# Kernel optimization log

Hardware: AMD Instinct MI355X
Metric: run time of the kernel (lower is better)

Reference implementation:

```python
import jax, jax.numpy as jnp
import numpy as np

V, E, H, K, B, T = 50000, 256, 128, 32, 64, 512


def lstm_dir(x, Wih, Whh, b, reverse):
    # x: [B,T,D]; torch gate order i,f,g,o
    Bsz = x.shape[0]
    xs = jnp.einsum('btd,gd->btg', x, Wih) + b  # [B,T,4H] precomputed input proj
    xs = jnp.swapaxes(xs, 0, 1)                 # [T,B,4H]
    def step(carry, xt):
        h, c = carry
        g = xt + h @ Whh.T
        i, f, gg, o = jnp.split(g, 4, axis=-1)
        c = jax.nn.sigmoid(f) * c + jax.nn.sigmoid(i) * jnp.tanh(gg)
        h = jax.nn.sigmoid(o) * jnp.tanh(c)
        return (h, c), h
    init = (jnp.zeros((Bsz, H), x.dtype), jnp.zeros((Bsz, H), x.dtype))
    _, hs = jax.lax.scan(step, init, xs, reverse=reverse)
    return jnp.swapaxes(hs, 0, 1)  # [B,T,H], time order preserved


def bilstm(x, layer_params):
    h = x
    for (Wf, Uf, bf, Wb, Ub, bb) in layer_params:
        fwd = lstm_dir(h, Wf, Uf, bf, False)
        bwd = lstm_dir(h, Wb, Ub, bb, True)
        h = jnp.concatenate([fwd, bwd], axis=-1)
    return h  # [B,T,2H]


def crf_nll(emissions, tags, mask, trans, start, end):
    Bsz, Tlen, Kn = emissions.shape
    maskf = mask.astype(emissions.dtype)
    # --- forward algorithm (log partition) ---
    alpha0 = start[None, :] + emissions[:, 0]  # [B,K]
    def step(alpha, xt):
        emit_t, m_t = xt  # [B,K], [B]
        score = alpha[:, :, None] + trans[None, :, :] + emit_t[:, None, :]  # [B,K,K]
        new = jax.nn.logsumexp(score, axis=1)
        alpha = jnp.where(m_t[:, None], new, alpha)
        return alpha, None
    em_t = jnp.swapaxes(emissions[:, 1:], 0, 1)  # [T-1,B,K]
    mk_t = jnp.swapaxes(mask[:, 1:], 0, 1)       # [T-1,B]
    alpha, _ = jax.lax.scan(step, alpha0, (em_t, mk_t))
    logZ = jax.nn.logsumexp(alpha + end[None, :], axis=1)  # [B]
    # --- gold path score ---
    emit = jnp.take_along_axis(emissions, tags[:, :, None].astype(jnp.int32), axis=2)[..., 0]  # [B,T]
    tr = trans[tags[:, 1:], tags[:, :-1]]  # [B,T-1]
    gold = start[tags[:, 0]] + emit[:, 0] + jnp.sum((emit[:, 1:] + tr) * maskf[:, 1:], axis=1)
    last = mask.astype(jnp.int32).sum(1) - 1
    last_tags = jnp.take_along_axis(tags, last[:, None], axis=1)[:, 0]
    gold = gold + end[last_tags]
    return jnp.mean(logZ - gold)


def setup_inputs() -> dict:
    key = jax.random.key(0)
    ks = jax.random.split(key, 24)
    s = 1.0 / np.sqrt(H)
    u = lambda k, sh, sc: jax.random.uniform(k, sh, jnp.float32, -sc, sc)
    inp = {}
    inp['x'] = jax.random.randint(ks[0], (B, T), 1, V, dtype=jnp.int32)  # avoid pad_idx 0
    inp['lens'] = jnp.full((B,), T, dtype=jnp.int32)
    inp['tags'] = jax.random.randint(ks[1], (B, T), 0, K, dtype=jnp.int32)
    inp['mask'] = jnp.ones((B, T), dtype=bool)
    emb = jax.random.normal(ks[2], (V, E), jnp.float32) * 0.1
    inp['emb'] = emb.at[0].set(0.0)  # padding_idx row
    d_in = [E, 2 * H]
    i = 3
    for l in range(2):
        for dname in ('f', 'b'):
            inp[f'Wih_l{l}{dname}'] = u(ks[i], (4 * H, d_in[l]), s); i += 1
            inp[f'Whh_l{l}{dname}'] = u(ks[i], (4 * H, H), s); i += 1
            inp[f'b_l{l}{dname}'] = u(ks[i], (4 * H,), s); i += 1  # bih+bhh combined
    inp['fcW'] = u(ks[i], (K, 2 * H), 1.0 / np.sqrt(2 * H)); i += 1
    inp['fcb'] = u(ks[i], (K,), 1.0 / np.sqrt(2 * H)); i += 1
    inp['trans'] = jax.random.normal(ks[i + 1], (K, K), jnp.float32) * 0.01
    inp['start'] = jax.random.normal(ks[i + 2], (K,), jnp.float32) * 0.01
    inp['end'] = jax.random.normal(ks[i + 3], (K,), jnp.float32) * 0.01
    return inp


def reference(x, lens, tags, mask, emb,
              Wih_l0f, Whh_l0f, b_l0f, Wih_l0b, Whh_l0b, b_l0b,
              Wih_l1f, Whh_l1f, b_l1f, Wih_l1b, Whh_l1b, b_l1b,
              fcW, fcb, trans, start, end):
    layer_params = [(Wih_l0f, Whh_l0f, b_l0f, Wih_l0b, Whh_l0b, b_l0b),
                    (Wih_l1f, Whh_l1f, b_l1f, Wih_l1b, Whh_l1b, b_l1b)]
    e = emb[x]                      # [B,T,E]
    o = bilstm(e, layer_params)     # [B,T,2H] (dropout: eval mode -> identity)
    emissions = o @ fcW.T + fcb     # [B,T,K]
    return crf_nll(emissions, tags, mask, trans, start, end)
```

## Files before the change

kernel.cpp:

```cpp
#include <hip/hip_runtime.h>
#include <stddef.h>

typedef unsigned short u16;
typedef unsigned int u32;

#define DEV __device__ __forceinline__

constexpr int Bb = 64;
constexpr int Tt = 512;
constexpr int Ee = 256;
constexpr int Hh = 128;
constexpr int Kk = 32;
constexpr int G4 = 4 * Hh;
constexpr int BT = Bb * Tt;

DEV u16 f2b(float f) {
  u32 u = __builtin_bit_cast(u32, f);
  u += 0x7fffu + ((u >> 16) & 1u);
  return (u16)(u >> 16);
}
DEV float b2f(u16 v) { return __builtin_bit_cast(float, (u32)v << 16); }
DEV float rcp_(float x) { float r; asm("v_rcp_f32 %0, %1" : "=v"(r) : "v"(x)); return r; }
DEV float sigmoidf_(float x) { return rcp_(1.0f + __expf(-x)); }
DEV float tanhf_(float x) { return 1.0f - 2.0f * rcp_(1.0f + __expf(2.0f * x)); }

DEV void gload16(const void* g, void* l) {
  __builtin_amdgcn_global_load_lds(
      (const __attribute__((address_space(1))) void*)g,
      (__attribute__((address_space(3))) void*)l, 16, 0, 0);
}

DEV void lds_barrier() {
  asm volatile("s_waitcnt lgkmcnt(0)" ::: "memory");
  __builtin_amdgcn_sched_barrier(0);
  __builtin_amdgcn_s_barrier();
  __builtin_amdgcn_sched_barrier(0);
}

__global__ __launch_bounds__(256) void k_embprep(
    const int* __restrict__ x, const float* __restrict__ emb,
    u16* __restrict__ eout,
    const float* __restrict__ W0, const float* __restrict__ W1,
    const float* __restrict__ W2, const float* __restrict__ W3,
    u16* __restrict__ d0, u16* __restrict__ d1,
    u16* __restrict__ d2, u16* __restrict__ d3,
    const float* __restrict__ fcW, u16* __restrict__ fcwb,
    const float* __restrict__ bi0, const float* __restrict__ bi1,
    const float* __restrict__ bi2, const float* __restrict__ bi3,
    float* __restrict__ bias_p) {
  int blk = blockIdx.x, tid = threadIdx.x;
  if (blk < 8192) {
    int m = blk * 4 + (tid >> 6);
    int lane = tid & 63;
    int b = m & 63, t = m >> 6;
    int idx = x[b * Tt + t];
    float4 v = ((const float4*)(emb + (size_t)idx * Ee))[lane];
    uint2 p;
    p.x = (u32)f2b(v.x) | ((u32)f2b(v.y) << 16);
    p.y = (u32)f2b(v.z) | ((u32)f2b(v.w) << 16);
    ((uint2*)(eout + (size_t)m * Ee))[lane] = p;
    return;
  }
  blk -= 8192;
  if (blk < 512) {
    int a = blk >> 7;
    const float* s; u16* d;
    if (a == 0)      { s = W0; d = d0; }
    else if (a == 1) { s = W1; d = d1; }
    else if (a == 2) { s = W2; d = d2; }
    else             { s = W3; d = d3; }
    int i = (blk & 127) * 256 + tid;
    int np = i >> 6, k4 = i & 63;
    int src = (np & 3) * 128 + (np >> 2);
    float4 v = ((const float4*)(s + (size_t)src * 256))[k4];
    uint2 p;
    p.x = (u32)f2b(v.x) | ((u32)f2b(v.y) << 16);
    p.y = (u32)f2b(v.z) | ((u32)f2b(v.w) << 16);
    ((uint2*)(d + (size_t)np * 256))[k4] = p;
  } else if (blk < 520) {
    int i = (blk - 512) * 256 + tid;
    float4 v = ((const float4*)fcW)[i];
    uint2 p;
    p.x = (u32)f2b(v.x) | ((u32)f2b(v.y) << 16);
    p.y = (u32)f2b(v.z) | ((u32)f2b(v.w) << 16);
    ((uint2*)fcwb)[i] = p;
  } else {
    int i = (blk - 520) * 256 + tid;
    int a = i >> 9, np = i & 511;
    const float* s;
    if (a == 0)      s = bi0;
    else if (a == 1) s = bi1;
    else if (a == 2) s = bi2;
    else             s = bi3;
    bias_p[i] = s[(np & 3) * 128 + (np >> 2)];
  }
}

typedef __attribute__((ext_vector_type(8))) short bfrag;
typedef __attribute__((ext_vector_type(4))) float ffrag;

__global__ __launch_bounds__(256) void k_gemm5(const u16* __restrict__ X,
                                               const u16* __restrict__ Wp0,
                                               const u16* __restrict__ Wp1,
                                               const float* __restrict__ bp0,
                                               const float* __restrict__ bp1,
                                               u16* __restrict__ out0,
                                               u16* __restrict__ out1) {
  __shared__ __align__(16) u16 Xs[128 * 64];
  __shared__ __align__(16) u16 Ws[128 * 64];
  const int tid = threadIdx.x;
  const int bm = blockIdx.x * 128;
  const int sel = blockIdx.y >> 2;
  const int bnp = (blockIdx.y & 3) * 128;
  const u16* __restrict__ Wp = sel ? Wp1 : Wp0;
  const float* __restrict__ bp = sel ? bp1 : bp0;
  u16* __restrict__ outp = sel ? out1 : out0;
  const int w = tid >> 6;
  const int l = tid & 63;
  const int r16 = l & 15;
  const int q = l >> 4;
  const int wrN = (w >> 1) * 64;
  const int wcM = (w & 1) * 64;

  const int srow = l >> 3;
  const int scol = l & 7;

  ffrag acc[4][4];
#pragma unroll
  for (int i = 0; i < 4; ++i)
#pragma unroll
    for (int jn = 0; jn < 4; ++jn) acc[i][jn] = (ffrag)0.0f;

  for (int kt = 0; kt < 256; kt += 64) {
#pragma unroll
    for (int i = 0; i < 4; ++i) {
      int row = w * 32 + i * 8 + srow;
      int gcol = (scol ^ (row & 7)) << 3;
      gload16(&X[(size_t)(bm + row) * 256 + kt + gcol], &Xs[(w * 32 + i * 8) * 64]);
      gload16(&Wp[(size_t)(bnp + row) * 256 + kt + gcol], &Ws[(w * 32 + i * 8) * 64]);
    }
    __syncthreads();
#pragma unroll
    for (int kk = 0; kk < 2; ++kk) {
      bfrag af[4], bf[4];
#pragma unroll
      for (int fm = 0; fm < 4; ++fm) {
        int row = wrN + fm * 16 + r16;
        int ck = (kk * 4 + q) ^ (row & 7);
        af[fm] = *(const bfrag*)&Ws[row * 64 + ck * 8];
      }
#pragma unroll
      for (int fn = 0; fn < 4; ++fn) {
        int row = wcM + fn * 16 + r16;
        int ck = (kk * 4 + q) ^ (row & 7);
        bf[fn] = *(const bfrag*)&Xs[row * 64 + ck * 8];
      }
#pragma unroll
      for (int fm = 0; fm < 4; ++fm)
#pragma unroll
        for (int fn = 0; fn < 4; ++fn)
          acc[fm][fn] = __builtin_amdgcn_mfma_f32_16x16x32_bf16(
              af[fm], bf[fn], acc[fm][fn], 0, 0, 0);
    }
    __syncthreads();
  }
  const int Q = l >> 4;
#pragma unroll
  for (int fm = 0; fm < 4; ++fm) {
    int np0 = bnp + wrN + fm * 16 + 4 * Q;
    int j = np0 >> 2;
    float4 bv = *(const float4*)&bp[np0];
#pragma unroll
    for (int fn = 0; fn < 4; ++fn) {
      int m = bm + wcM + fn * 16 + r16;
      int t = m >> 6, bq = (m & 63) >> 2;
      size_t flat = ((size_t)t * 16 + bq) * 2048 + (size_t)j * 16 + (m & 3) * 4;
      float v0 = acc[fm][fn][0] + bv.x, v1 = acc[fm][fn][1] + bv.y;
      float v2 = acc[fm][fn][2] + bv.z, v3 = acc[fm][fn][3] + bv.w;
      u32 lo, hi;
      asm("v_cvt_pk_bf16_f32 %0, %1, %2" : "=v"(lo) : "v"(v0), "v"(v1));
      asm("v_cvt_pk_bf16_f32 %0, %1, %2" : "=v"(hi) : "v"(v2), "v"(v3));
      uint2 st; st.x = lo; st.y = hi;
      *(uint2*)&outp[flat] = st;
    }
  }
}

__global__ __launch_bounds__(512, 1) void k_lstm9(const u16* __restrict__ xpf,
                                                  const u16* __restrict__ xpb,
                                                  const float* __restrict__ whhf,
                                                  const float* __restrict__ whhb,
                                                  u16* __restrict__ out) {
  __shared__ u16 hbuf[2][4][128];
  const int dir = blockIdx.x >> 4;
  const int wg = blockIdx.x & 15;
  const u16* __restrict__ xp = dir ? xpb : xpf;
  const float* __restrict__ whh = dir ? whhb : whhf;
  const int tid = threadIdx.x;
  const int w = tid >> 6;
  const int l = tid & 63;
  const int q = l >> 4;
  const int jw = l & 15;
  const int j = 16 * w + jw;

  for (int i = tid; i < 2 * 4 * 128; i += 512) (&hbuf[0][0][0])[i] = 0;

  bfrag wf[4][4];
#pragma unroll
  for (int g = 0; g < 4; ++g) {
    const float* rowp = whh + (size_t)(g * 128 + j) * 128;
#pragma unroll
    for (int ks = 0; ks < 4; ++ks) {
      float4 x0 = ((const float4*)(rowp + ks * 32 + q * 8))[0];
      float4 x1 = ((const float4*)(rowp + ks * 32 + q * 8))[1];
      bfrag t;
      t[0] = (short)f2b(x0.x); t[1] = (short)f2b(x0.y);
      t[2] = (short)f2b(x0.z); t[3] = (short)f2b(x0.w);
      t[4] = (short)f2b(x1.x); t[5] = (short)f2b(x1.y);
      t[6] = (short)f2b(x1.z); t[7] = (short)f2b(x1.w);
      wf[g][ks] = t;
    }
  }
  __syncthreads();

  const int dt = dir ? -1 : 1;
  const int tp0 = dir ? (Tt - 1) : 0;
  const size_t xoff = (size_t)wg * 2048 + (size_t)j * 16 + (size_t)q * 4;
  float cc = 0.f;
  int cur = 0;
  u16 hprev = 0;

  const bool ld_act = ((jw & 3) == 0);
  const int drow = jw >> 2;
  const int rsw = (drow & 1) << 5;
  const int wsw = (q & 1) << 5;
  bfrag hf0 = (bfrag)(short)0, hf1 = (bfrag)(short)0;
  bfrag hf2 = (bfrag)(short)0, hf3 = (bfrag)(short)0;

  uint2 xv[4];
#pragma unroll
  for (int d = 0; d < 4; ++d)
    xv[d] = *(const uint2*)&xp[(size_t)(tp0 + d * dt) * 32768 + xoff];

  const ptrdiff_t xstep = (ptrdiff_t)dt * 32768;
  const u16* pxq = xp + (size_t)(tp0 + 4 * dt) * 32768 + xoff;
  u16* optr = out + ((size_t)tp0 * 64 + 4 * wg + q) * 256 + (size_t)dir * 128 + j;
  const ptrdiff_t ostep = (ptrdiff_t)dt * 16384;

  for (int it = 0; it < Tt / 4; ++it) {
#pragma unroll
    for (int d = 0; d < 4; ++d) {
      if (it > 0 || d > 0) { *optr = hprev; optr += ostep; }

      if (ld_act) {
        const u16* hb = &hbuf[cur][drow][0];
        hf0 = *(const bfrag*)&hb[(0 * 32 + q * 8) ^ rsw];
        hf1 = *(const bfrag*)&hb[(1 * 32 + q * 8) ^ rsw];
        hf2 = *(const bfrag*)&hb[(2 * 32 + q * 8) ^ rsw];
        hf3 = *(const bfrag*)&hb[(3 * 32 + q * 8) ^ rsw];
      }

      ffrag a0 = __builtin_amdgcn_mfma_f32_16x16x32_bf16(hf0, wf[0][0], (ffrag)0.f, 0, 0, 0);
      ffrag a1 = __builtin_amdgcn_mfma_f32_16x16x32_bf16(hf0, wf[1][0], (ffrag)0.f, 0, 0, 0);
      ffrag a2 = __builtin_amdgcn_mfma_f32_16x16x32_bf16(hf0, wf[2][0], (ffrag)0.f, 0, 0, 0);
      ffrag a3 = __builtin_amdgcn_mfma_f32_16x16x32_bf16(hf0, wf[3][0], (ffrag)0.f, 0, 0, 0);
      a0 = __builtin_amdgcn_mfma_f32_16x16x32_bf16(hf1, wf[0][1], a0, 0, 0, 0);
      a1 = __builtin_amdgcn_mfma_f32_16x16x32_bf16(hf1, wf[1][1], a1, 0, 0, 0);
      a2 = __builtin_amdgcn_mfma_f32_16x16x32_bf16(hf1, wf[2][1], a2, 0, 0, 0);
      a3 = __builtin_amdgcn_mfma_f32_16x16x32_bf16(hf1, wf[3][1], a3, 0, 0, 0);
      a0 = __builtin_amdgcn_mfma_f32_16x16x32_bf16(hf2, wf[0][2], a0, 0, 0, 0);
      a1 = __builtin_amdgcn_mfma_f32_16x16x32_bf16(hf2, wf[1][2], a1, 0, 0, 0);
      a2 = __builtin_amdgcn_mfma_f32_16x16x32_bf16(hf2, wf[2][2], a2, 0, 0, 0);
      a3 = __builtin_amdgcn_mfma_f32_16x16x32_bf16(hf2, wf[3][2], a3, 0, 0, 0);
      a0 = __builtin_amdgcn_mfma_f32_16x16x32_bf16(hf3, wf[0][3], a0, 0, 0, 0);
      a1 = __builtin_amdgcn_mfma_f32_16x16x32_bf16(hf3, wf[1][3], a1, 0, 0, 0);
      a2 = __builtin_amdgcn_mfma_f32_16x16x32_bf16(hf3, wf[2][3], a2, 0, 0, 0);
      a3 = __builtin_amdgcn_mfma_f32_16x16x32_bf16(hf3, wf[3][3], a3, 0, 0, 0);

      float gi = a0[0] + b2f((u16)xv[d].x);
      float gf = a1[0] + b2f((u16)(xv[d].x >> 16));
      float gg = a2[0] + b2f((u16)xv[d].y);
      float go = a3[0] + b2f((u16)(xv[d].y >> 16));
      cc = sigmoidf_(gf) * cc + sigmoidf_(gi) * tanhf_(gg);
      float h = sigmoidf_(go) * tanhf_(cc);
      u16 hv = f2b(h);

      hbuf[cur ^ 1][q][j ^ wsw] = hv;
      hprev = hv;

      xv[d] = *(const uint2*)pxq;
      pxq += xstep;

      lds_barrier();
      cur ^= 1;
    }
  }
  *optr = hprev;
}

__global__ __launch_bounds__(256) void k_fc2(const u16* __restrict__ X,
                                             const u16* __restrict__ Wc,
                                             const float* __restrict__ bias,
                                             float* __restrict__ emis) {
  constexpr int LDT = 72;
  __shared__ u16 Xs[128 * LDT];
  __shared__ u16 Ws[32 * LDT];
  const int tid = threadIdx.x;
  const int bm = blockIdx.x * 128;
  const int w = tid >> 6;
  const int l = tid & 63;
  const int r16 = l & 15;
  const int k8 = (l >> 4) << 3;

  ffrag acc[2][2];
#pragma unroll
  for (int i = 0; i < 2; ++i)
#pragma unroll
    for (int jn = 0; jn < 2; ++jn) acc[i][jn] = (ffrag)0.0f;

  for (int kt = 0; kt < 256; kt += 64) {
#pragma unroll
    for (int c = 0; c < 4; ++c) {
      int ch = tid + 256 * c;
      int row = ch >> 3, c8 = (ch & 7) << 3;
      *(uint4*)&Xs[row * LDT + c8] =
          *(const uint4*)&X[(size_t)(bm + row) * 256 + kt + c8];
    }
    {
      int row = tid >> 3, c8 = (tid & 7) << 3;
      *(uint4*)&Ws[row * LDT + c8] =
          *(const uint4*)&Wc[(size_t)row * 256 + kt + c8];
    }
    __syncthreads();
#pragma unroll
    for (int kk = 0; kk < 2; ++kk) {
      bfrag af[2], bf[2];
#pragma unroll
      for (int fm = 0; fm < 2; ++fm)
        af[fm] = *(const bfrag*)&Xs[(32 * w + fm * 16 + r16) * LDT + kk * 32 + k8];
#pragma unroll
      for (int fn = 0; fn < 2; ++fn)
        bf[fn] = *(const bfrag*)&Ws[(fn * 16 + r16) * LDT + kk * 32 + k8];
#pragma unroll
      for (int fm = 0; fm < 2; ++fm)
#pragma unroll
        for (int fn = 0; fn < 2; ++fn)
          acc[fm][fn] = __builtin_amdgcn_mfma_f32_16x16x32_bf16(
              af[fm], bf[fn], acc[fm][fn], 0, 0, 0);
    }
    __syncthreads();
  }
  const int rbase = (l >> 4) * 4;
#pragma unroll
  for (int fm = 0; fm < 2; ++fm)
#pragma unroll
    for (int fn = 0; fn < 2; ++fn) {
      int cj = fn * 16 + r16;
      float bv = bias[cj];
#pragma unroll
      for (int r = 0; r < 4; ++r) {
        int m = bm + 32 * w + fm * 16 + rbase + r;
        emis[(size_t)m * Kk + cj] = acc[fm][fn][r] + bv;
      }
    }
}

__global__ __launch_bounds__(64) void k_crf(const float* __restrict__ emis,
                                            const int* __restrict__ tags,
                                            const float* __restrict__ trans,
                                            const float* __restrict__ startv,
                                            const float* __restrict__ endv,
                                            float* __restrict__ nll) {
  __shared__ float tr[Kk * Kk];
  const int b = blockIdx.x;
  const int l = threadIdx.x;
  const int j = l & 31;
  const int half = l >> 5;
  for (int i = l; i < Kk * Kk; i += 64) tr[i] = trans[i];
  float E_r[16];
#pragma unroll
  for (int i = 0; i < 16; ++i) E_r[i] = __expf(trans[(half * 16 + i) * Kk + j]);
  const float* eb = emis + (size_t)b * Kk;
  float aj = startv[j] + eb[j];
  float ebc = eb[2048 + j];
  __syncthreads();

  for (int t = 1; t < Tt; ++t) {
    float ebn = eb[(size_t)(t + 1) * 2048 + j];
    float m = aj;
    m = fmaxf(m, __shfl_xor(m, 16));
    m = fmaxf(m, __shfl_xor(m, 8));
    m = fmaxf(m, __shfl_xor(m, 4));
    m = fmaxf(m, __shfl_xor(m, 2));
    m = fmaxf(m, __shfl_xor(m, 1));
    float p = __expf(aj - m);
    float c0 = 0.f, c1 = 0.f, c2 = 0.f, c3 = 0.f;
#pragma unroll
    for (int i = 0; i < 16; i += 4) {
      c0 = fmaf(__shfl(p, half * 16 + i),     E_r[i],     c0);
      c1 = fmaf(__shfl(p, half * 16 + i + 1), E_r[i + 1], c1);
      c2 = fmaf(__shfl(p, half * 16 + i + 2), E_r[i + 2], c2);
      c3 = fmaf(__shfl(p, half * 16 + i + 3), E_r[i + 3], c3);
    }
    float s = (c0 + c1) + (c2 + c3);
    s += __shfl_xor(s, 32);
    aj = ebc + m + __logf(s);
    ebc = ebn;
  }

  float val = aj + endv[j];
  float M = val;
#pragma unroll
  for (int off = 16; off > 0; off >>= 1) M = fmaxf(M, __shfl_xor(M, off));
  float sz = __expf(val - M);
#pragma unroll
  for (int off = 16; off > 0; off >>= 1) sz += __shfl_xor(sz, off);
  float logZ = M + __logf(sz);

  const int* tg = tags + (size_t)b * Tt;
  float g = 0.f;
  for (int t = l; t < Tt; t += 64) {
    int cur = tg[t];
    g += eb[(size_t)t * 2048 + cur];
    if (t >= 1) g += tr[cur * Kk + tg[t - 1]];
  }
#pragma unroll
  for (int off = 32; off > 0; off >>= 1) g += __shfl_xor(g, off);
  if (l == 0) {
    g += startv[tg[0]] + endv[tg[Tt - 1]];
    nll[b] = logZ - g;
  }
}

__global__ void k_reduce(const float* __restrict__ nll, float* __restrict__ out) {
  float v = nll[threadIdx.x];
#pragma unroll
  for (int off = 32; off > 0; off >>= 1) v += __shfl_xor(v, off);
  if (threadIdx.x == 0) out[0] = v * (1.0f / 64.0f);
}

extern "C" void kernel_launch(void* const* d_in, const int* in_sizes, int n_in,
                              void* d_out, int out_size, void* d_ws, size_t ws_size,
                              hipStream_t stream) {
  (void)in_sizes; (void)n_in; (void)out_size; (void)ws_size;
  const int*   x      = (const int*)d_in[0];
  const int*   tags   = (const int*)d_in[2];
  const float* emb    = (const float*)d_in[4];
  const float* Wih0f  = (const float*)d_in[5];
  const float* Whh0f  = (const float*)d_in[6];
  const float* b0f    = (const float*)d_in[7];
  const float* Wih0b  = (const float*)d_in[8];
  const float* Whh0b  = (const float*)d_in[9];
  const float* b0b    = (const float*)d_in[10];
  const float* Wih1f  = (const float*)d_in[11];
  const float* Whh1f  = (const float*)d_in[12];
  const float* b1f    = (const float*)d_in[13];
  const float* Wih1b  = (const float*)d_in[14];
  const float* Whh1b  = (const float*)d_in[15];
  const float* b1b    = (const float*)d_in[16];
  const float* fcW    = (const float*)d_in[17];
  const float* fcb    = (const float*)d_in[18];
  const float* trans  = (const float*)d_in[19];
  const float* startv = (const float*)d_in[20];
  const float* endv   = (const float*)d_in[21];

  char* p = (char*)d_ws;
  u16* buf0 = (u16*)p; p += (size_t)BT * Ee * 2;
  u16* buf1 = (u16*)p; p += (size_t)BT * 256 * 2;
  u16* xpf  = (u16*)p; p += (size_t)BT * G4 * 2;
  u16* xpb  = (u16*)p; p += (size_t)BT * G4 * 2;
  u16* wb[4];
  for (int i = 0; i < 4; ++i) { wb[i] = (u16*)p; p += (size_t)512 * 256 * 2; }
  u16* fcwb = (u16*)p; p += (size_t)32 * 256 * 2;
  float* bias_p = (float*)p; p += 4 * 512 * 4;
  float* emis = (float*)p; p += ((size_t)BT * Kk + 64 * Kk) * 4;
  float* nll  = (float*)p; p += 256;

  k_embprep<<<dim3(8192 + 528), dim3(256), 0, stream>>>(
      x, emb, buf0,
      Wih0f, Wih0b, Wih1f, Wih1b, wb[0], wb[1], wb[2], wb[3],
      fcW, fcwb, b0f, b0b, b1f, b1b, bias_p);

  dim3 ggrid(BT / 128, 8);
  k_gemm5<<<ggrid, dim3(256), 0, stream>>>(buf0, wb[0], wb[1],
                                           bias_p, bias_p + 512, xpf, xpb);
  k_lstm9<<<dim3(32), dim3(512), 0, stream>>>(xpf, xpb, Whh0f, Whh0b, buf1);
  k_gemm5<<<ggrid, dim3(256), 0, stream>>>(buf1, wb[2], wb[3],
                                           bias_p + 1024, bias_p + 1536, xpf, xpb);
  k_lstm9<<<dim3(32), dim3(512), 0, stream>>>(xpf, xpb, Whh1f, Whh1b, buf0);
  k_fc2<<<dim3(BT / 128), dim3(256), 0, stream>>>(buf0, fcwb, fcb, emis);
  k_crf<<<dim3(Bb), dim3(64), 0, stream>>>(emis, tags, trans, startv, endv, nll);
  k_reduce<<<dim3(1), dim3(64), 0, stream>>>(nll, (float*)d_out);
}
```

Baseline: 757.1 us.

## Prescale LSTM gates by log2e, enlarge GEMM tile, lazily refresh CRF max

```diff
diff --git a/kernel.cpp b/kernel.cpp
--- a/kernel.cpp
+++ b/kernel.cpp
@@ -13,6 +13,7 @@
 constexpr int Kk = 32;
 constexpr int G4 = 4 * Hh;
 constexpr int BT = Bb * Tt;
+constexpr float L2E = 1.44269504f;
 
 DEV u16 f2b(float f) {
   u32 u = __builtin_bit_cast(u32, f);
@@ -21,8 +22,7 @@
 }
 DEV float b2f(u16 v) { return __builtin_bit_cast(float, (u32)v << 16); }
 DEV float rcp_(float x) { float r; asm("v_rcp_f32 %0, %1" : "=v"(r) : "v"(x)); return r; }
-DEV float sigmoidf_(float x) { return rcp_(1.0f + __expf(-x)); }
-DEV float tanhf_(float x) { return 1.0f - 2.0f * rcp_(1.0f + __expf(2.0f * x)); }
+DEV float exp2_(float x) { float r; asm("v_exp_f32 %0, %1" : "=v"(r) : "v"(x)); return r; }
 
 DEV void gload16(const void* g, void* l) {
   __builtin_amdgcn_global_load_lds(
@@ -74,8 +74,8 @@
     int src = (np & 3) * 128 + (np >> 2);
     float4 v = ((const float4*)(s + (size_t)src * 256))[k4];
     uint2 p;
-    p.x = (u32)f2b(v.x) | ((u32)f2b(v.y) << 16);
-    p.y = (u32)f2b(v.z) | ((u32)f2b(v.w) << 16);
+    p.x = (u32)f2b(v.x * L2E) | ((u32)f2b(v.y * L2E) << 16);
+    p.y = (u32)f2b(v.z * L2E) | ((u32)f2b(v.w * L2E) << 16);
     ((uint2*)(d + (size_t)np * 256))[k4] = p;
   } else if (blk < 520) {
     int i = (blk - 512) * 256 + tid;
@@ -92,24 +92,24 @@
     else if (a == 1) s = bi1;
     else if (a == 2) s = bi2;
     else             s = bi3;
-    bias_p[i] = s[(np & 3) * 128 + (np >> 2)];
+    bias_p[i] = s[(np & 3) * 128 + (np >> 2)] * L2E;
   }
 }
 
 typedef __attribute__((ext_vector_type(8))) short bfrag;
 typedef __attribute__((ext_vector_type(4))) float ffrag;
 
-__global__ __launch_bounds__(256) void k_gemm5(const u16* __restrict__ X,
+__global__ __launch_bounds__(512) void k_gemm6(const u16* __restrict__ X,
                                                const u16* __restrict__ Wp0,
                                                const u16* __restrict__ Wp1,
                                                const float* __restrict__ bp0,
                                                const float* __restrict__ bp1,
                                                u16* __restrict__ out0,
                                                u16* __restrict__ out1) {
-  __shared__ __align__(16) u16 Xs[128 * 64];
+  __shared__ __align__(16) u16 Xs[256 * 64];
   __shared__ __align__(16) u16 Ws[128 * 64];
   const int tid = threadIdx.x;
-  const int bm = blockIdx.x * 128;
+  const int bm = blockIdx.x * 256;
   const int sel = blockIdx.y >> 2;
   const int bnp = (blockIdx.y & 3) * 128;
   const u16* __restrict__ Wp = sel ? Wp1 : Wp0;
@@ -119,9 +119,8 @@
   const int l = tid & 63;
   const int r16 = l & 15;
   const int q = l >> 4;
-  const int wrN = (w >> 1) * 64;
-  const int wcM = (w & 1) * 64;
-
+  const int wrN = (w >> 2) * 64;
+  const int wcM = (w & 3) * 64;
   const int srow = l >> 3;
   const int scol = l & 7;
 
@@ -135,9 +134,14 @@
 #pragma unroll
     for (int i = 0; i < 4; ++i) {
       int row = w * 32 + i * 8 + srow;
-      int gcol = (scol ^ (row & 7)) << 3;
+      int gcol = (scol ^ (srow & 7)) << 3;
       gload16(&X[(size_t)(bm + row) * 256 + kt + gcol], &Xs[(w * 32 + i * 8) * 64]);
-      gload16(&Wp[(size_t)(bnp + row) * 256 + kt + gcol], &Ws[(w * 32 + i * 8) * 64]);
+    }
+#pragma unroll
+    for (int i = 0; i < 2; ++i) {
+      int row = w * 16 + i * 8 + srow;
+      int gcol = (scol ^ (srow & 7)) << 3;
+      gload16(&Wp[(size_t)(bnp + row) * 256 + kt + gcol], &Ws[(w * 16 + i * 8) * 64]);
     }
     __syncthreads();
 #pragma unroll
@@ -186,11 +190,11 @@
   }
 }
 
-__global__ __launch_bounds__(512, 1) void k_lstm9(const u16* __restrict__ xpf,
-                                                  const u16* __restrict__ xpb,
-                                                  const float* __restrict__ whhf,
-                                                  const float* __restrict__ whhb,
-                                                  u16* __restrict__ out) {
+__global__ __launch_bounds__(512, 1) void k_lstm10(const u16* __restrict__ xpf,
+                                                   const u16* __restrict__ xpb,
+                                                   const float* __restrict__ whhf,
+                                                   const float* __restrict__ whhb,
+                                                   u16* __restrict__ out) {
   __shared__ u16 hbuf[2][4][128];
   const int dir = blockIdx.x >> 4;
   const int wg = blockIdx.x & 15;
@@ -214,10 +218,10 @@
       float4 x0 = ((const float4*)(rowp + ks * 32 + q * 8))[0];
       float4 x1 = ((const float4*)(rowp + ks * 32 + q * 8))[1];
       bfrag t;
-      t[0] = (short)f2b(x0.x); t[1] = (short)f2b(x0.y);
-      t[2] = (short)f2b(x0.z); t[3] = (short)f2b(x0.w);
-      t[4] = (short)f2b(x1.x); t[5] = (short)f2b(x1.y);
-      t[6] = (short)f2b(x1.z); t[7] = (short)f2b(x1.w);
+      t[0] = (short)f2b(x0.x * L2E); t[1] = (short)f2b(x0.y * L2E);
+      t[2] = (short)f2b(x0.z * L2E); t[3] = (short)f2b(x0.w * L2E);
+      t[4] = (short)f2b(x1.x * L2E); t[5] = (short)f2b(x1.y * L2E);
+      t[6] = (short)f2b(x1.z * L2E); t[7] = (short)f2b(x1.w * L2E);
       wf[g][ks] = t;
     }
   }
@@ -281,8 +285,13 @@
       float gf = a1[0] + b2f((u16)(xv[d].x >> 16));
       float gg = a2[0] + b2f((u16)xv[d].y);
       float go = a3[0] + b2f((u16)(xv[d].y >> 16));
-      cc = sigmoidf_(gf) * cc + sigmoidf_(gi) * tanhf_(gg);
-      float h = sigmoidf_(go) * tanhf_(cc);
+      float sf = rcp_(1.0f + exp2_(-gf));
+      float si = rcp_(1.0f + exp2_(-gi));
+      float tg = 1.0f - 2.0f * rcp_(1.0f + exp2_(gg + gg));
+      float so = rcp_(1.0f + exp2_(-go));
+      cc = sf * cc + si * tg;
+      float th = 1.0f - 2.0f * rcp_(1.0f + exp2_(2.88539008f * cc));
+      float h = so * th;
       u16 hv = f2b(h);
 
       hbuf[cur ^ 1][q][j ^ wsw] = hv;
@@ -385,14 +394,20 @@
   float ebc = eb[2048 + j];
   __syncthreads();
 
+  float m = aj;
+#pragma unroll
+  for (int off = 16; off > 0; off >>= 1) m = fmaxf(m, __shfl_xor(m, off));
+
   for (int t = 1; t < Tt; ++t) {
     float ebn = eb[(size_t)(t + 1) * 2048 + j];
-    float m = aj;
-    m = fmaxf(m, __shfl_xor(m, 16));
-    m = fmaxf(m, __shfl_xor(m, 8));
-    m = fmaxf(m, __shfl_xor(m, 4));
-    m = fmaxf(m, __shfl_xor(m, 2));
-    m = fmaxf(m, __shfl_xor(m, 1));
+    if (__any(aj - m > 30.0f)) {
+      m = aj;
+      m = fmaxf(m, __shfl_xor(m, 16));
+      m = fmaxf(m, __shfl_xor(m, 8));
+      m = fmaxf(m, __shfl_xor(m, 4));
+      m = fmaxf(m, __shfl_xor(m, 2));
+      m = fmaxf(m, __shfl_xor(m, 1));
+    }
     float p = __expf(aj - m);
     float c0 = 0.f, c1 = 0.f, c2 = 0.f, c3 = 0.f;
 #pragma unroll
@@ -481,13 +496,13 @@
       Wih0f, Wih0b, Wih1f, Wih1b, wb[0], wb[1], wb[2], wb[3],
       fcW, fcwb, b0f, b0b, b1f, b1b, bias_p);
 
-  dim3 ggrid(BT / 128, 8);
-  k_gemm5<<<ggrid, dim3(256), 0, stream>>>(buf0, wb[0], wb[1],
+  dim3 ggrid(BT / 256, 8);
+  k_gemm6<<<ggrid, dim3(512), 0, stream>>>(buf0, wb[0], wb[1],
                                            bias_p, bias_p + 512, xpf, xpb);
-  k_lstm9<<<dim3(32), dim3(512), 0, stream>>>(xpf, xpb, Whh0f, Whh0b, buf1);
-  k_gemm5<<<ggrid, dim3(256), 0, stream>>>(buf1, wb[2], wb[3],
+  k_lstm10<<<dim3(32), dim3(512), 0, stream>>>(xpf, xpb, Whh0f, Whh0b, buf1);
+  k_gemm6<<<ggrid, dim3(512), 0, stream>>>(buf1, wb[2], wb[3],
                                            bias_p + 1024, bias_p + 1536, xpf, xpb);
-  k_lstm9<<<dim3(32), dim3(512), 0, stream>>>(xpf, xpb, Whh1f, Whh1b, buf0);
+  k_lstm10<<<dim3(32), dim3(512), 0, stream>>>(xpf, xpb, Whh1f, Whh1b, buf0);
   k_fc2<<<dim3(BT / 128), dim3(256), 0, stream>>>(buf0, fcwb, fcb, emis);
   k_crf<<<dim3(Bb), dim3(64), 0, stream>>>(emis, tags, trans, startv, endv, nll);
   k_reduce<<<dim3(1), dim3(64), 0, stream>>>(nll, (float*)d_out);
```

Result: faster. 709.0 us (-6.4%).
